# Optimization experiments

Measured on AMD Instinct MI355X. Metric: run time of the kernel, lower is better.

Reference implementation:

```python
import jax, jax.numpy as jnp
import numpy as np

N, C, L = 1024, 3, 6000
CONV_CH = [20, 32, 64, 20]
K = 3            # conv kernel size, padding (K-1)//2 = 1 -> SAME
POOL = 2
HID = 100
FLAT_DIM = (L // POOL**4 + 2 * C + 1) * CONV_CH[-1]  # (375 + 7) * 20 = 7640


def setup_inputs() -> dict:
    key = jax.random.key(0)
    ks = jax.random.split(key, 10)
    d = {"x": jax.random.normal(ks[0], (N, C, L), jnp.float32)}
    ins = [C] + CONV_CH[:-1]
    for i, (ic, oc) in enumerate(zip(ins, CONV_CH)):
        d[f"w{i}"] = jax.random.normal(ks[1 + i], (oc, ic, K), jnp.float32) * (1.0 / np.sqrt(ic * K))
        d[f"b{i}"] = jnp.zeros((oc,), jnp.float32)
    d["wc"] = jax.random.normal(ks[6], (CONV_CH[-1], C, 1), jnp.float32) * (1.0 / np.sqrt(C))
    d["bc"] = jnp.zeros((CONV_CH[-1],), jnp.float32)
    d["wl0"] = jax.random.normal(ks[7], (HID, FLAT_DIM), jnp.float32) * (1.0 / np.sqrt(FLAT_DIM))
    d["bl0"] = jnp.zeros((HID,), jnp.float32)
    d["wl1"] = jax.random.normal(ks[8], (2, HID), jnp.float32) * (1.0 / np.sqrt(HID))
    d["bl1"] = jnp.zeros((2,), jnp.float32)
    return d


def conv1d(x, w, b, pad):
    # x: (N, C_in, L), w: (C_out, C_in, K)
    out = jax.lax.conv_general_dilated(x, w, (1,), [(pad, pad)],
                                       dimension_numbers=('NCH', 'OIH', 'NCH'))
    return out + b[None, :, None]


def maxpool2(x):
    n, c, l = x.shape  # l always even here (6000 / 2^k)
    return x.reshape(n, c, l // 2, 2).max(-1)


def cov_eig_feats(x):
    # batched covariance as a single contraction (avoids the O(N*L*C*C) bmm intermediate)
    n, c, l = x.shape
    diff = x - x.mean(-1, keepdims=True)
    cov = jnp.einsum('ncl,ndl->ncd', diff, diff) / (l - 1)  # (N, C, C)
    # cov is symmetric PSD -> eigh (real); torch uses generic eig and keeps real parts
    vals, vecs = jnp.linalg.eigh(cov)
    vals = vals[..., None] / vals.max()          # global max over batch, like torch
    cov = cov / jnp.abs(cov).max()
    return jnp.concatenate([cov, vals, vecs], axis=-1)  # (N, C, 2C+1)


def reference(x, w0, b0, w1, b1, w2, b2, w3, b3, wc, bc, wl0, bl0, wl1, bl1):
    feats = jax.lax.stop_gradient(cov_eig_feats(x))  # torch branch is @no_grad
    h = x
    for w, b in ((w0, b0), (w1, b1), (w2, b2), (w3, b3)):
        h = maxpool2(jax.nn.relu(conv1d(h, w, b, (K - 1) // 2)))
    h = h.reshape(h.shape[0], -1)                    # (N, 20*375)
    h1 = jax.nn.relu(conv1d(feats, wc, bc, 0))       # (N, 20, 7)
    h1 = h1.reshape(h1.shape[0], -1)
    h = jnp.concatenate([h, h1], axis=1)             # (N, 7640)
    h = jax.nn.relu(h @ wl0.T + bl0)
    out = h @ wl1.T + bl1                            # (N, 2)
    return (out[:, :1], out[:, 1:])
```

## Files before the change

### kernel.cpp

```cpp
#include <hip/hip_runtime.h>
#include <hip/hip_bf16.h>
#include <hip/hip_fp16.h>
#include <math.h>

#define NBATCH 1024
#define LIN    6000
#define HCATW  7640
#define HID    100

#define TCH   54
#define NCHK  7

#define ASZ 3552
#define BSZ 7040

#define W0OFF 0
#define W1OFF 192
#define W2OFF 1472
#define W3OFF 5568
#define B0OFF 9664
#define B1OFF 9684
#define B2OFF 9716
#define B3OFF 9780
#define WREPSZ 9800

#define FCNS 4

typedef _Float16 v2h __attribute__((ext_vector_type(2)));

__device__ __forceinline__ float fdot2_f16(unsigned int a, unsigned int b, float c) {
#if __has_builtin(__builtin_amdgcn_fdot2)
    v2h ah, bh;
    __builtin_memcpy(&ah, &a, 4);
    __builtin_memcpy(&bh, &b, 4);
    return __builtin_amdgcn_fdot2(ah, bh, c, false);
#else
    float d;
    asm("v_dot2_f32_f16 %0, %1, %2, %3" : "=v"(d) : "v"(a), "v"(b), "v"(c));
    return d;
#endif
}

__device__ __forceinline__ void pack_one(int idx, int OC, int IC, int OCG,
                                         int OPG, int WSTR,
                                         const float* __restrict__ w,
                                         float* __restrict__ dst)
{
    if (idx >= OCG * IC * WSTR) return;
    int ocg = idx / (IC * WSTR);
    int r   = idx - ocg * (IC * WSTR);
    int ic  = r / WSTR;
    int q   = r - ic * WSTR;
    int o   = q / 3, k = q - o * 3;
    int oc  = ocg * OPG + o;
    dst[idx] = (o < OPG && oc < OC) ? w[(oc * IC + ic) * 3 + k] : 0.f;
}

__device__ __forceinline__ void pack_pk(int idx, int OC, int IC,
                                        const float* __restrict__ w,
                                        unsigned int* __restrict__ dst)
{
    const int OCG = OC >> 3;
    if (idx >= OCG * IC * 16) return;
    int ocg = idx / (IC * 16);
    int r   = idx - ocg * (IC * 16);
    int ic  = r >> 4, q = r & 15;
    int o   = q & 7;
    int oc  = ocg * 8 + o;
    const float* ws = w + (oc * IC + ic) * 3;
    if (q < 8) {
        unsigned int lo = __half_as_ushort(__float2half(ws[0]));
        unsigned int hi = __half_as_ushort(__float2half(ws[1]));
        dst[idx] = lo | (hi << 16);
    } else {
        dst[idx] = __float_as_uint(ws[2]);
    }
}

__global__ __launch_bounds__(256) void repack_kernel(
    const float* __restrict__ w0, const float* __restrict__ b0,
    const float* __restrict__ w1, const float* __restrict__ b1,
    const float* __restrict__ w2, const float* __restrict__ b2,
    const float* __restrict__ w3, const float* __restrict__ b3,
    float* __restrict__ wrep)
{
    int idx = blockIdx.x * 256 + threadIdx.x;
    unsigned int* wu = (unsigned int*)wrep;
    pack_one(idx, 20,  3, 4, 5, 16, w0, wrep + W0OFF);
    pack_pk (idx, 32, 20, w1, wu + W1OFF);
    pack_pk (idx, 64, 32, w2, wu + W2OFF);
    pack_one(idx, 20, 64, 4, 5, 16, w3, wrep + W3OFF);
    if (idx < 20)            wrep[B0OFF + idx] = b0[idx];
    else if (idx < 52)  { int i = idx - 20;  wrep[B1OFF + i] = b1[i]; }
    else if (idx < 116) { int i = idx - 52;  wrep[B2OFF + i] = b2[i]; }
    else if (idx < 136) { int i = idx - 116; wrep[B3OFF + i] = b3[i]; }
}

template<int IC, int OC, int OCG, int OPG, int WSTR, int JOUT, int LG, int JBLK,
         bool IN16, bool OUT16, bool PKW, bool FINAL>
__device__ __forceinline__ void stage_eo(const float* __restrict__ in,
                                         float* __restrict__ out,
                                         float* __restrict__ outg,
                                         const float* __restrict__ wrep,
                                         const float* __restrict__ brep,
                                         int pbase, int o3, int wv, int lane,
                                         int zero)
{
    constexpr int PIN  = JOUT + 1;
    constexpr int POUT = JOUT / 2;
    constexpr int NJT  = (JOUT + 64 * JBLK - 1) / (64 * JBLK);
    for (int task = wv; task < OCG * NJT; task += 8) {
        const int ocg = task / NJT;
        const int jt  = task - ocg * NJT;
        const int j0  = jt * (64 * JBLK) + lane;
        const float* bp = brep + ocg * OPG;
        float ae[JBLK][OPG], ao[JBLK][OPG];
#pragma unroll
        for (int t = 0; t < JBLK; ++t)
#pragma unroll
            for (int o = 0; o < OPG; ++o) { ae[t][o] = bp[o]; ao[t][o] = ae[t][o]; }
        const float* wbase = wrep + ocg * (IC * WSTR) + zero;
#pragma unroll 2
        for (int ic = 0; ic < IC; ++ic) {
            const float* wp = wbase + ic * WSTR;
            float wr[WSTR];
#pragma unroll
            for (int q = 0; q < WSTR / 4; ++q)
                *(float4*)&wr[q * 4] = *(const float4*)(wp + q * 4);
#pragma unroll
            for (int t = 0; t < JBLK; ++t) {
                const int jj = j0 + t * 64;
                const int jc = (jj < JOUT) ? jj : (JOUT - 1);
                if constexpr (PKW) {
                    const float* ipw = in + ic * PIN;
                    uint2 pw;
                    __builtin_memcpy(&pw, ipw + jc, 8);
                    const unsigned int crossu = (pw.x >> 16) | (pw.y << 16);
                    v2h h1; __builtin_memcpy(&h1, &pw.y, 4);
                    const float e1 = (float)h1.x, o1 = (float)h1.y;
#pragma unroll
                    for (int o = 0; o < OPG; ++o) {
                        const unsigned int wpk = __float_as_uint(wr[o]);
                        const float w2 = wr[8 + o];
                        ae[t][o] = fdot2_f16(pw.x,  wpk, ae[t][o]);
                        ao[t][o] = fdot2_f16(crossu, wpk, ao[t][o]);
                        ae[t][o] = fmaf(e1, w2, ae[t][o]);
                        ao[t][o] = fmaf(o1, w2, ao[t][o]);
                    }
                } else {
                    float e0, e1, o0, o1;
                    if constexpr (IN16) {
                        const float* ipw = in + ic * PIN;
                        uint2 pw;
                        __builtin_memcpy(&pw, ipw + jc, 8);
                        __half2 h0 = *reinterpret_cast<const __half2*>(&pw.x);
                        __half2 h1 = *reinterpret_cast<const __half2*>(&pw.y);
                        e0 = __low2float(h0); o0 = __high2float(h0);
                        e1 = __low2float(h1); o1 = __high2float(h1);
                    } else {
                        const float* ip = in + ic * (2 * PIN);
                        float2 ev, ov;
                        __builtin_memcpy(&ev, ip + jc, 8);
                        __builtin_memcpy(&ov, ip + PIN + jc, 8);
                        e0 = ev.x; e1 = ev.y;
                        o0 = ov.x; o1 = ov.y;
                    }
#pragma unroll
                    for (int o = 0; o < OPG; ++o) {
                        const float w0 = wr[o*3+0], w1 = wr[o*3+1], w2 = wr[o*3+2];
                        ae[t][o] = fmaf(e0, w0, fmaf(o0, w1, fmaf(e1, w2, ae[t][o])));
                        ao[t][o] = fmaf(o0, w0, fmaf(e1, w1, fmaf(o1, w2, ao[t][o])));
                    }
                }
            }
        }
#pragma unroll
        for (int t = 0; t < JBLK; ++t) {
            const int jj = j0 + t * 64;
            if constexpr (FINAL) {
                const int gj = o3 + jj;
                if (gj < 375 && jj < JOUT) {
#pragma unroll
                    for (int o = 0; o < OPG; ++o)
                        outg[(ocg*OPG+o) * 375 + gj] =
                            fmaxf(fmaxf(ae[t][o], ao[t][o]), 0.f);
                }
            } else {
                const int g = pbase + jj;
                const bool val = (jj < JOUT) && (g >= 0) && (g < LG);
                if (jj < JOUT) {
                    if constexpr (OUT16) {
                        __half* dh = (__half*)out;
#pragma unroll
                        for (int o = 0; o < OPG; ++o) {
                            float v = val ? fmaxf(fmaxf(ae[t][o], ao[t][o]), 0.f)
                                          : 0.f;
                            dh[(ocg*OPG+o) * JOUT + jj] = __float2half(v);
                        }
                    } else {
                        float* dst = out + ((jj & 1) ? POUT : 0) + (jj >> 1);
#pragma unroll
                        for (int o = 0; o < OPG; ++o)
                            dst[(ocg*OPG+o) * JOUT] =
                                val ? fmaxf(fmaxf(ae[t][o], ao[t][o]), 0.f) : 0.f;
                    }
                }
            }
        }
    }
}

__device__ __forceinline__ void stage3_split(const float* __restrict__ in,
                                             float* __restrict__ part,
                                             float* __restrict__ outg,
                                             const float* __restrict__ wrep,
                                             const float* __restrict__ brep,
                                             int o3, int wv, int lane, int zero)
{
    constexpr int JOUT = 54, PIN = 55, OPG = 5, WSTR = 16;
    const int ocg = wv & 3, ih = wv >> 2;
    const int j  = lane;
    const int jc = (j < JOUT) ? j : (JOUT - 1);
    const float* bp = brep + ocg * OPG;
    float ae[OPG], ao[OPG];
#pragma unroll
    for (int o = 0; o < OPG; ++o) {
        float b = ih ? 0.f : bp[o];
        ae[o] = b; ao[o] = b;
    }
    const float* wbase = wrep + (ocg * 64 + ih * 32) * WSTR + zero;
#pragma unroll 2
    for (int ic = 0; ic < 32; ++ic) {
        const float* ip = in + (ih * 32 + ic) * (2 * PIN);
        float2 ev, ov;
        __builtin_memcpy(&ev, ip + jc, 8);
        __builtin_memcpy(&ov, ip + PIN + jc, 8);
        const float* wp = wbase + ic * WSTR;
        float wr[WSTR];
#pragma unroll
        for (int q = 0; q < WSTR / 4; ++q)
            *(float4*)&wr[q * 4] = *(const float4*)(wp + q * 4);
#pragma unroll
        for (int o = 0; o < OPG; ++o) {
            const float w0 = wr[o*3+0], w1 = wr[o*3+1], w2 = wr[o*3+2];
            ae[o] = fmaf(ev.x, w0, fmaf(ov.x, w1, fmaf(ev.y, w2, ae[o])));
            ao[o] = fmaf(ov.x, w0, fmaf(ev.y, w1, fmaf(ov.y, w2, ao[o])));
        }
    }
    if (ih == 1) {
#pragma unroll
        for (int o = 0; o < OPG; ++o) {
            float2 p = make_float2(ae[o], ao[o]);
            __builtin_memcpy(part + (ocg * OPG + o) * 128 + lane * 2, &p, 8);
        }
    }
    __syncthreads();
    if (ih == 0) {
#pragma unroll
        for (int o = 0; o < OPG; ++o) {
            float2 p;
            __builtin_memcpy(&p, part + (ocg * OPG + o) * 128 + lane * 2, 8);
            ae[o] += p.x; ao[o] += p.y;
        }
        const int gj = o3 + j;
        if (gj < 375 && j < JOUT) {
#pragma unroll
            for (int o = 0; o < OPG; ++o)
                outg[(ocg * OPG + o) * 375 + gj] =
                    fmaxf(fmaxf(ae[o], ao[o]), 0.f);
        }
    }
}

__global__ __launch_bounds__(512, 6) void conv_chain_eo(
    const float* __restrict__ x,
    const float* __restrict__ wrep,
    float* __restrict__ hcat)
{
    __shared__ float A[ASZ];
    __shared__ float B[BSZ];

    const int tid  = threadIdx.x;
    const int wv   = __builtin_amdgcn_readfirstlane(tid >> 6);
    const int lane = tid & 63;
    const int zero = __builtin_amdgcn_ds_bpermute(0, 0);
    const int n     = blockIdx.x / NCHK;
    const int chunk = blockIdx.x % NCHK;
    const int o3 = chunk * TCH;
    const int p2 = 2*o3 - 1, p1 = 4*o3 - 3, p0 = 8*o3 - 7, xs = 16*o3 - 15;

    const float* xn = x + (size_t)n * 3 * LIN;
    for (int idx = tid; idx < 3 * 894; idx += 512) {
        int c = idx / 894, i = idx - c * 894;
        int g = xs + i;
        float v = (g >= 0 && g < LIN) ? xn[c * LIN + g] : 0.f;
        A[c * 894 + ((i & 1) ? 447 : 0) + (i >> 1)] = v;
    }
    __syncthreads();
    stage_eo< 3, 20, 4, 5, 16, 446, 3000, 2, false, true,  false, false>(
        A, B, nullptr, wrep + W0OFF, wrep + B0OFF, p0, o3, wv, lane, zero);
    __syncthreads();
    stage_eo<20, 32, 4, 8, 16, 222, 1500, 2, true,  true,  true,  false>(
        B, A, nullptr, wrep + W1OFF, wrep + B1OFF, p1, o3, wv, lane, zero);
    __syncthreads();
    stage_eo<32, 64, 8, 8, 16, 110,  750, 2, true,  false, true,  false>(
        A, B, nullptr, wrep + W2OFF, wrep + B2OFF, p2, o3, wv, lane, zero);
    __syncthreads();
    stage3_split(B, A, hcat + (size_t)n * HCATW,
                 wrep + W3OFF, wrep + B3OFF, o3, wv, lane, zero);
}

__device__ __forceinline__ float fsign(float a, float b) {
    return (b >= 0.0f) ? fabsf(a) : -fabsf(a);
}
__device__ __forceinline__ float slapy2(float xx, float yy) {
    float xa = fabsf(xx), ya = fabsf(yy);
    float w = fmaxf(xa, ya), z = fminf(xa, ya);
    if (z == 0.f) return w;
    float t = z / w;
    return w * sqrtf(1.f + t*t);
}
__device__ __forceinline__ void slartg(float f, float g, float& c, float& s, float& r) {
    if (g == 0.f)      { c = 1.f; s = 0.f; r = f; }
    else if (f == 0.f) { c = 0.f; s = (g >= 0.f ? 1.f : -1.f); r = fabsf(g); }
    else {
        float d = sqrtf(f*f + g*g);
        c = fabsf(f) / d;
        r = fsign(d, f);
        s = g / r;
    }
}
__device__ void slaev2(float a, float b, float cc,
                       float& rt1, float& rt2, float& cs1, float& sn1) {
    float sm = a + cc, df = a - cc;
    float adf = fabsf(df);
    float tb = b + b, ab = fabsf(tb);
    float acmx, acmn;
    if (fabsf(a) > fabsf(cc)) { acmx = a; acmn = cc; } else { acmx = cc; acmn = a; }
    float rt;
    if (adf > ab)      { float t = ab/adf; rt = adf*sqrtf(1.f + t*t); }
    else if (adf < ab) { float t = adf/ab; rt = ab*sqrtf(1.f + t*t); }
    else rt = ab * sqrtf(2.f);
    int sgn1;
    if (sm < 0.f)      { rt1 = 0.5f*(sm - rt); sgn1 = -1; rt2 = (acmx/rt1)*acmn - (b/rt1)*b; }
    else if (sm > 0.f) { rt1 = 0.5f*(sm + rt); sgn1 =  1; rt2 = (acmx/rt1)*acmn - (b/rt1)*b; }
    else               { rt1 = 0.5f*rt; rt2 = -0.5f*rt; sgn1 = 1; }
    float cs; int sgn2;
    if (df >= 0.f) { cs = df + rt; sgn2 = 1; } else { cs = df - rt; sgn2 = -1; }
    float acs = fabsf(cs);
    if (acs > ab) {
        float ct = -tb / cs;
        sn1 = 1.f / sqrtf(1.f + ct*ct);
        cs1 = ct * sn1;
    } else {
        if (ab == 0.f) { cs1 = 1.f; sn1 = 0.f; }
        else {
            float tn = -cs / tb;
            cs1 = 1.f / sqrtf(1.f + tn*tn);
            sn1 = tn * cs1;
        }
    }
    if (sgn1 == sgn2) { float tn = cs1; cs1 = -sn1; sn1 = tn; }
}
__device__ __forceinline__ void rot_cols(float z[3][3], int jc, float c, float s) {
    for (int i = 0; i < 3; ++i) {
        float t = z[i][jc+1];
        z[i][jc+1] = c*t - s*z[i][jc];
        z[i][jc]   = s*t + c*z[i][jc];
    }
}

__device__ void ssteqr3(float d[3], float e[2], float z[3][3]) {
    const float eps    = 5.9604645e-8f;
    const float eps2   = eps * eps;
    const float safmin = 1.17549435e-38f;
    const int n = 3;
    for (int i = 0; i < 3; ++i)
        for (int j = 0; j < 3; ++j) z[i][j] = (i == j) ? 1.f : 0.f;
    const int nmaxit = n * 30;
    int jtot = 0;
    float cw[2], sw[2];
    int l1 = 1, l, m, lend, lsv, lendsv;

L10:
    if (l1 > n) goto L160;
    if (l1 > 1) e[l1-2] = 0.f;
    if (l1 <= n-1) {
        for (m = l1; m <= n-1; ++m) {
            float tst = fabsf(e[m-1]);
            if (tst == 0.f) goto L30;
            if (tst <= (sqrtf(fabsf(d[m-1])) * sqrtf(fabsf(d[m]))) * eps) {
                e[m-1] = 0.f;
                goto L30;
            }
        }
    }
    m = n;
L30:
    l = l1; lsv = l; lend = m; lendsv = lend; l1 = m + 1;
    if (lend == l) goto L10;
    if (fabsf(d[lend-1]) < fabsf(d[l-1])) { lend = lsv; l = lendsv; }
    if (lend > l) {
L40:
        if (l != lend) {
            bool found = false;
            for (m = l; m <= lend-1; ++m) {
                float tst = e[m-1]*e[m-1];
                if (tst <= (eps2*fabsf(d[m-1]))*fabsf(d[m]) + safmin) { found = true; break; }
            }
            if (!found) m = lend;
        } else m = lend;
        if (m < lend) e[m-1] = 0.f;
        {
            float p = d[l-1];
            if (m == l) {
                d[l-1] = p;
                l = l + 1;
                if (l <= lend) goto L40;
                goto L140;
            }
            if (m == l+1) {
                float rt1, rt2, c2, s2;
                slaev2(d[l-1], e[l-1], d[l], rt1, rt2, c2, s2);
                rot_cols(z, l-1, c2, s2);
                d[l-1] = rt1; d[l] = rt2; e[l-1] = 0.f;
                l += 2;
                if (l <= lend) goto L40;
                goto L140;
            }
            if (jtot == nmaxit) goto L140;
            jtot++;
            float g = (d[l] - p) / (2.f * e[l-1]);
            float r = slapy2(g, 1.f);
            g = d[m-1] - p + e[l-1] / (g + fsign(r, g));
            float s = 1.f, c = 1.f;
            p = 0.f;
            for (int i = m-1; i >= l; --i) {
                float f = s * e[i-1];
                float b = c * e[i-1];
                slartg(g, f, c, s, r);
                if (i != m-1) e[i] = r;
                g = d[i] - p;
                r = (d[i-1] - g)*s + 2.f*c*b;
                p = s * r;
                d[i] = g + p;
                g = c*r - b;
                cw[i-l] = c; sw[i-l] = -s;
            }
            for (int jj = m-l; jj >= 1; --jj)
                rot_cols(z, l + jj - 2, cw[jj-1], sw[jj-1]);
            d[l-1] = d[l-1] - p;
            e[l-1] = g;
            goto L40;
        }
    } else {
L90:
        if (l != lend) {
            bool found = false;
            for (m = l; m >= lend+1; --m) {
                float tst = e[m-2]*e[m-2];
                if (tst <= (eps2*fabsf(d[m-1]))*fabsf(d[m-2]) + safmin) { found = true; break; }
            }
            if (!found) m = lend;
        } else m = lend;
        if (m > lend) e[m-2] = 0.f;
        {
            float p = d[l-1];
            if (m == l) {
                d[l-1] = p;
                l = l - 1;
                if (l >= lend) goto L90;
                goto L140;
            }
            if (m == l-1) {
                float rt1, rt2, c2, s2;
                slaev2(d[l-2], e[l-2], d[l-1], rt1, rt2, c2, s2);
                rot_cols(z, l-2, c2, s2);
                d[l-2] = rt1; d[l-1] = rt2; e[l-2] = 0.f;
                l -= 2;
                if (l >= lend) goto L90;
                goto L140;
            }
            if (jtot == nmaxit) goto L140;
            jtot++;
            float g = (d[l-2] - p) / (2.f * e[l-2]);
            float r = slapy2(g, 1.f);
            g = d[m-1] - p + e[l-2] / (g + fsign(r, g));
            float s = 1.f, c = 1.f;
            p = 0.f;
            for (int i = m; i <= l-1; ++i) {
                float f = s * e[i-1];
                float b = c * e[i-1];
                slartg(g, f, c, s, r);
                if (i != m) e[i-2] = r;
                g = d[i-1] - p;
                r = (d[i] - g)*s + 2.f*c*b;
                p = s * r;
                d[i-1] = g + p;
                g = c*r - b;
                cw[i-m] = c; sw[i-m] = s;
            }
            for (int jj = 1; jj <= l-m; ++jj)
                rot_cols(z, m + jj - 2, cw[jj-1], sw[jj-1]);
            d[l-1] = d[l-1] - p;
            e[l-2] = g;
            goto L90;
        }
    }
L140:
    if (jtot < nmaxit) goto L10;
L160:
    for (int ii = 2; ii <= n; ++ii) {
        int i = ii - 1, k = i;
        float p = d[i-1];
        for (int j = ii; j <= n; ++j)
            if (d[j-1] < p) { k = j; p = d[j-1]; }
        if (k != i) {
            d[k-1] = d[i-1]; d[i-1] = p;
            for (int r0 = 0; r0 < 3; ++r0) {
                float t = z[r0][i-1]; z[r0][i-1] = z[r0][k-1]; z[r0][k-1] = t;
            }
        }
    }
}

__global__ __launch_bounds__(256) void cov_eig_kernel(const float* __restrict__ x,
                                                      float* __restrict__ eigbuf,
                                                      unsigned int* __restrict__ gmax)
{
    __shared__ float part[4][9];
    const int n = blockIdx.x;
    const float* xn = x + (size_t)n * 3 * LIN;
    float v[9] = {0,0,0,0,0,0,0,0,0};
    for (int l = threadIdx.x; l < LIN; l += 256) {
        float a = xn[l], b = xn[LIN + l], c = xn[2*LIN + l];
        v[0] += a; v[1] += b; v[2] += c;
        v[3] = fmaf(a,a,v[3]); v[4] = fmaf(a,b,v[4]); v[5] = fmaf(a,c,v[5]);
        v[6] = fmaf(b,b,v[6]); v[7] = fmaf(b,c,v[7]); v[8] = fmaf(c,c,v[8]);
    }
#pragma unroll
    for (int off = 32; off > 0; off >>= 1)
#pragma unroll
        for (int i = 0; i < 9; ++i) v[i] += __shfl_down(v[i], off, 64);
    const int wv = threadIdx.x >> 6, lane = threadIdx.x & 63;
    if (lane == 0)
        for (int i = 0; i < 9; ++i) part[wv][i] = v[i];
    __syncthreads();
    if (threadIdx.x == 0) {
        float t[9];
        for (int i = 0; i < 9; ++i)
            t[i] = part[0][i] + part[1][i] + part[2][i] + part[3][i];
        const float Lf = (float)LIN;
        float m0 = t[0]/Lf, m1 = t[1]/Lf, m2 = t[2]/Lf;
        float c00 = (t[3] - Lf*m0*m0) / (Lf - 1.f);
        float c01 = (t[4] - Lf*m0*m1) / (Lf - 1.f);
        float c02 = (t[5] - Lf*m0*m2) / (Lf - 1.f);
        float c11 = (t[6] - Lf*m1*m1) / (Lf - 1.f);
        float c12 = (t[7] - Lf*m1*m2) / (Lf - 1.f);
        float c22 = (t[8] - Lf*m2*m2) / (Lf - 1.f);

        float dd[3], ee[2], tau, v2;
        {
            float a21 = c01, a31 = c02, a22 = c11, a32 = c12, a33 = c22;
            float xnorm = fabsf(a31);
            if (xnorm == 0.f) {
                tau = 0.f; v2 = 0.f;
                dd[0] = c00; dd[1] = a22; dd[2] = a33;
                ee[0] = a21; ee[1] = a32;
            } else {
                float beta = -fsign(slapy2(a21, xnorm), a21);
                tau = (beta - a21) / beta;
                v2  = a31 / (a21 - beta);
                ee[0] = beta;
                float x1 = tau*(a22 + a32*v2);
                float x2 = tau*(a32 + a33*v2);
                float al = -0.5f*tau*(x1 + x2*v2);
                float w1 = x1 + al;
                float w2 = x2 + al*v2;
                a22 -= 2.f*w1;
                a32 -= (v2*w1 + w2);
                a33 -= 2.f*v2*w2;
                dd[0] = c00; dd[1] = a22; dd[2] = a33;
                ee[1] = a32;
            }
        }
        float zz[3][3];
        ssteqr3(dd, ee, zz);
        if (tau != 0.f) {
            for (int j = 0; j < 3; ++j) {
                float sum = zz[1][j] + v2*zz[2][j];
                zz[1][j] -= tau * sum;
                zz[2][j] -= tau * v2 * sum;
            }
        }

        float* eb = eigbuf + n * 21;
        eb[0] = c00; eb[1] = c01; eb[2] = c02;
        eb[3] = c01; eb[4] = c11; eb[5] = c12;
        eb[6] = c02; eb[7] = c12; eb[8] = c22;
        eb[9] = dd[0]; eb[10] = dd[1]; eb[11] = dd[2];
        for (int c = 0; c < 3; ++c)
            for (int k = 0; k < 3; ++k) eb[12 + c*3 + k] = zz[c][k];

        float vmax = fmaxf(dd[0], fmaxf(dd[1], dd[2]));
        float cmax = 0.f;
        for (int i = 0; i < 9; ++i) cmax = fmaxf(cmax, fabsf(eb[i]));
        atomicMax(&gmax[0], __float_as_uint(vmax));
        atomicMax(&gmax[1], __float_as_uint(cmax));
    }
}

__global__ __launch_bounds__(256) void feats_kernel(const float* __restrict__ eigbuf,
                                                    const unsigned int* __restrict__ gmax,
                                                    const float* __restrict__ wc,
                                                    const float* __restrict__ bc,
                                                    float* __restrict__ hcat)
{
    const int n = blockIdx.x;
    const int t = threadIdx.x;
    if (t >= 140) return;
    const int o = t / 7, j = t % 7;
    const float* eb = eigbuf + n * 21;
    const float vmax = __uint_as_float(gmax[0]);
    const float cmax = __uint_as_float(gmax[1]);
    float f0, f1, f2;
    if (j < 3)       { f0 = eb[0*3+j]/cmax; f1 = eb[1*3+j]/cmax; f2 = eb[2*3+j]/cmax; }
    else if (j == 3) { f0 = eb[9]/vmax;     f1 = eb[10]/vmax;    f2 = eb[11]/vmax; }
    else             { int k = j-4; f0 = eb[12+0*3+k]; f1 = eb[12+1*3+k]; f2 = eb[12+2*3+k]; }
    float r = bc[o] + wc[o*3+0]*f0 + wc[o*3+1]*f1 + wc[o*3+2]*f2;
    hcat[(size_t)n*HCATW + 7500 + o*7 + j] = fmaxf(r, 0.f);
}

__global__ __launch_bounds__(512) void fc01_kernel(const float* __restrict__ hcat,
                                                   const float* __restrict__ wl0,
                                                   const float* __restrict__ bl0,
                                                   const float* __restrict__ wl1,
                                                   const float* __restrict__ bl1,
                                                   float* __restrict__ out)
{
    __shared__ float hl[FCNS * HCATW];
    __shared__ float hbuf[FCNS * HID];
    const int tid = threadIdx.x;
    const int n0 = blockIdx.x * FCNS;
    for (int i = tid; i < FCNS * (HCATW/4); i += 512) {
        int s  = i / (HCATW/4);
        int k4 = i - s * (HCATW/4);
        ((float4*)hl)[s * (HCATW/4) + k4] =
            *(const float4*)(hcat + (size_t)(n0 + s) * HCATW + k4 * 4);
    }
    __syncthreads();
    const int wv = tid >> 6;
    const int lane = tid & 63;
    for (int ot = wv; ot < HID / 4; ot += 8) {
        float acc[4][FCNS];
#pragma unroll
        for (int oo = 0; oo < 4; ++oo)
#pragma unroll
            for (int s = 0; s < FCNS; ++s) acc[oo][s] = 0.f;
        for (int k = lane * 4; k < HCATW; k += 256) {
            float4 hv[FCNS];
#pragma unroll
            for (int s = 0; s < FCNS; ++s)
                hv[s] = *(const float4*)(hl + s * HCATW + k);
#pragma unroll
            for (int oo = 0; oo < 4; ++oo) {
                const float4 w4 = *(const float4*)(wl0 + (size_t)(ot*4+oo) * HCATW + k);
#pragma unroll
                for (int s = 0; s < FCNS; ++s) {
                    acc[oo][s] = fmaf(hv[s].x, w4.x, acc[oo][s]);
                    acc[oo][s] = fmaf(hv[s].y, w4.y, acc[oo][s]);
                    acc[oo][s] = fmaf(hv[s].z, w4.z, acc[oo][s]);
                    acc[oo][s] = fmaf(hv[s].w, w4.w, acc[oo][s]);
                }
            }
        }
#pragma unroll
        for (int off = 32; off > 0; off >>= 1)
#pragma unroll
            for (int oo = 0; oo < 4; ++oo)
#pragma unroll
                for (int s = 0; s < FCNS; ++s)
                    acc[oo][s] += __shfl_down(acc[oo][s], off, 64);
        if (lane == 0) {
#pragma unroll
            for (int oo = 0; oo < 4; ++oo) {
                const float b = bl0[ot*4+oo];
#pragma unroll
                for (int s = 0; s < FCNS; ++s)
                    hbuf[s * HID + ot*4+oo] = fmaxf(acc[oo][s] + b, 0.f);
            }
        }
    }
    __syncthreads();
    if (tid < 2 * FCNS) {
        const int s = tid >> 1, r = tid & 1;
        const float* w = wl1 + r * HID;
        float acc = bl1[r];
        for (int k = 0; k < HID; ++k) acc = fmaf(hbuf[s * HID + k], w[k], acc);
        out[r * NBATCH + n0 + s] = acc;
    }
}

extern "C" void kernel_launch(void* const* d_in, const int* in_sizes, int n_in,
                              void* d_out, int out_size, void* d_ws, size_t ws_size,
                              hipStream_t stream)
{
    const float* x   = (const float*)d_in[0];
    const float* w0  = (const float*)d_in[1];
    const float* b0  = (const float*)d_in[2];
    const float* w1  = (const float*)d_in[3];
    const float* b1  = (const float*)d_in[4];
    const float* w2  = (const float*)d_in[5];
    const float* b2  = (const float*)d_in[6];
    const float* w3  = (const float*)d_in[7];
    const float* b3  = (const float*)d_in[8];
    const float* wc  = (const float*)d_in[9];
    const float* bc  = (const float*)d_in[10];
    const float* wl0 = (const float*)d_in[11];
    const float* bl0 = (const float*)d_in[12];
    const float* wl1 = (const float*)d_in[13];
    const float* bl1 = (const float*)d_in[14];
    float* out = (float*)d_out;

    const size_t HCAT_N = (size_t)NBATCH * HCATW;
    const size_t EIG_N  = (size_t)NBATCH * 21;
    const size_t need_bytes = (HCAT_N + EIG_N + 4 + WREPSZ) * 4 + 16;
    if (ws_size < need_bytes) return;

    float* ws     = (float*)d_ws;
    float* hcat   = ws;
    float* eigbuf = hcat + HCAT_N;
    unsigned int* gmax = (unsigned int*)(eigbuf + EIG_N);
    float* wrep   = (float*)(gmax + 4);

    hipMemsetAsync(gmax, 0, 2 * sizeof(unsigned int), stream);

    repack_kernel<<<16, 256, 0, stream>>>(w0, b0, w1, b1, w2, b2, w3, b3, wrep);
    conv_chain_eo<<<NBATCH * NCHK, 512, 0, stream>>>(x, wrep, hcat);
    cov_eig_kernel<<<NBATCH, 256, 0, stream>>>(x, eigbuf, gmax);
    feats_kernel<<<NBATCH, 256, 0, stream>>>(eigbuf, gmax, wc, bc, hcat);
    fc01_kernel<<<NBATCH / FCNS, 512, 0, stream>>>(hcat, wl0, bl0, wl1, bl1, out);
}
```

Before: 652.0 us.

## Use fp16 packed dot products for conv stage 3 and FC layer

Stage 2 now writes its output as packed fp16 into a smaller shared buffer, and stage 3 reads packed halves and uses v_dot2 with fp16-packed weights. The FC1 weights are converted to fp16 by a new per-call kernel, and the hidden activations are staged in shared memory as fp16. Batch rows per FC block double, so each weight load is reused across more samples. The smaller shared footprint lets the occupancy hint rise to 8 blocks per CU, at the cost of reduced precision in these layers.

Result: faster. 615.4 us (-5.6%).

```diff
diff --git a/kernel.cpp b/kernel.cpp
--- a/kernel.cpp
+++ b/kernel.cpp
@@ -12,7 +12,7 @@
 #define NCHK  7
 
 #define ASZ 3552
-#define BSZ 7040
+#define BSZ 4460
 
 #define W0OFF 0
 #define W1OFF 192
@@ -24,7 +24,9 @@
 #define B3OFF 9780
 #define WREPSZ 9800
 
-#define FCNS 4
+#define WL0HSZ (HID * (HCATW/2))
+
+#define FCNS 8
 
 typedef _Float16 v2h __attribute__((ext_vector_type(2)));
 
@@ -56,25 +58,29 @@
     dst[idx] = (o < OPG && oc < OC) ? w[(oc * IC + ic) * 3 + k] : 0.f;
 }
 
-__device__ __forceinline__ void pack_pk(int idx, int OC, int IC,
+__device__ __forceinline__ void pack_pk(int idx, int OC, int IC, int OCG, int OPG,
                                         const float* __restrict__ w,
                                         unsigned int* __restrict__ dst)
 {
-    const int OCG = OC >> 3;
     if (idx >= OCG * IC * 16) return;
     int ocg = idx / (IC * 16);
     int r   = idx - ocg * (IC * 16);
     int ic  = r >> 4, q = r & 15;
     int o   = q & 7;
-    int oc  = ocg * 8 + o;
-    const float* ws = w + (oc * IC + ic) * 3;
-    if (q < 8) {
-        unsigned int lo = __half_as_ushort(__float2half(ws[0]));
-        unsigned int hi = __half_as_ushort(__float2half(ws[1]));
-        dst[idx] = lo | (hi << 16);
-    } else {
-        dst[idx] = __float_as_uint(ws[2]);
-    }
+    int oc  = ocg * OPG + o;
+    bool valid = (o < OPG) && (oc < OC);
+    unsigned int v = 0;
+    if (valid) {
+        const float* ws = w + (oc * IC + ic) * 3;
+        if (q < 8) {
+            unsigned int lo = __half_as_ushort(__float2half(ws[0]));
+            unsigned int hi = __half_as_ushort(__float2half(ws[1]));
+            v = lo | (hi << 16);
+        } else {
+            v = __float_as_uint(ws[2]);
+        }
+    }
+    dst[idx] = v;
 }
 
 __global__ __launch_bounds__(256) void repack_kernel(
@@ -87,13 +93,24 @@
     int idx = blockIdx.x * 256 + threadIdx.x;
     unsigned int* wu = (unsigned int*)wrep;
     pack_one(idx, 20,  3, 4, 5, 16, w0, wrep + W0OFF);
-    pack_pk (idx, 32, 20, w1, wu + W1OFF);
-    pack_pk (idx, 64, 32, w2, wu + W2OFF);
-    pack_one(idx, 20, 64, 4, 5, 16, w3, wrep + W3OFF);
+    pack_pk (idx, 32, 20, 4, 8, w1, wu + W1OFF);
+    pack_pk (idx, 64, 32, 8, 8, w2, wu + W2OFF);
+    pack_pk (idx, 20, 64, 4, 5, w3, wu + W3OFF);
     if (idx < 20)            wrep[B0OFF + idx] = b0[idx];
     else if (idx < 52)  { int i = idx - 20;  wrep[B1OFF + i] = b1[i]; }
     else if (idx < 116) { int i = idx - 52;  wrep[B2OFF + i] = b2[i]; }
     else if (idx < 136) { int i = idx - 116; wrep[B3OFF + i] = b3[i]; }
+}
+
+__global__ __launch_bounds__(256) void wl0h_kernel(const float* __restrict__ wl0,
+                                                   unsigned int* __restrict__ wl0h)
+{
+    int idx = blockIdx.x * 256 + threadIdx.x;
+    if (idx >= WL0HSZ) return;
+    float a = wl0[idx * 2], b = wl0[idx * 2 + 1];
+    unsigned int lo = __half_as_ushort(__float2half(a));
+    unsigned int hi = __half_as_ushort(__float2half(b));
+    wl0h[idx] = lo | (hi << 16);
 }
 
 template<int IC, int OC, int OCG, int OPG, int WSTR, int JOUT, int LG, int JBLK,
@@ -217,7 +234,7 @@
                                              const float* __restrict__ brep,
                                              int o3, int wv, int lane, int zero)
 {
-    constexpr int JOUT = 54, PIN = 55, OPG = 5, WSTR = 16;
+    constexpr int JOUT = 54, PIND = 55, OPG = 5, WSTR = 16;
     const int ocg = wv & 3, ih = wv >> 2;
     const int j  = lane;
     const int jc = (j < JOUT) ? j : (JOUT - 1);
@@ -231,10 +248,12 @@
     const float* wbase = wrep + (ocg * 64 + ih * 32) * WSTR + zero;
 #pragma unroll 2
     for (int ic = 0; ic < 32; ++ic) {
-        const float* ip = in + (ih * 32 + ic) * (2 * PIN);
-        float2 ev, ov;
-        __builtin_memcpy(&ev, ip + jc, 8);
-        __builtin_memcpy(&ov, ip + PIN + jc, 8);
+        const float* ipw = in + (ih * 32 + ic) * PIND;
+        uint2 pw;
+        __builtin_memcpy(&pw, ipw + jc, 8);
+        const unsigned int crossu = (pw.x >> 16) | (pw.y << 16);
+        v2h h1; __builtin_memcpy(&h1, &pw.y, 4);
+        const float e1 = (float)h1.x, o1 = (float)h1.y;
         const float* wp = wbase + ic * WSTR;
         float wr[WSTR];
 #pragma unroll
@@ -242,9 +261,12 @@
             *(float4*)&wr[q * 4] = *(const float4*)(wp + q * 4);
 #pragma unroll
         for (int o = 0; o < OPG; ++o) {
-            const float w0 = wr[o*3+0], w1 = wr[o*3+1], w2 = wr[o*3+2];
-            ae[o] = fmaf(ev.x, w0, fmaf(ov.x, w1, fmaf(ev.y, w2, ae[o])));
-            ao[o] = fmaf(ov.x, w0, fmaf(ev.y, w1, fmaf(ov.y, w2, ao[o])));
+            const unsigned int wpk = __float_as_uint(wr[o]);
+            const float w2 = wr[8 + o];
+            ae[o] = fdot2_f16(pw.x,   wpk, ae[o]);
+            ao[o] = fdot2_f16(crossu, wpk, ao[o]);
+            ae[o] = fmaf(e1, w2, ae[o]);
+            ao[o] = fmaf(o1, w2, ao[o]);
         }
     }
     if (ih == 1) {
@@ -272,7 +294,7 @@
     }
 }
 
-__global__ __launch_bounds__(512, 6) void conv_chain_eo(
+__global__ __launch_bounds__(512, 8) void conv_chain_eo(
     const float* __restrict__ x,
     const float* __restrict__ wrep,
     float* __restrict__ hcat)
@@ -303,7 +325,7 @@
     stage_eo<20, 32, 4, 8, 16, 222, 1500, 2, true,  true,  true,  false>(
         B, A, nullptr, wrep + W1OFF, wrep + B1OFF, p1, o3, wv, lane, zero);
     __syncthreads();
-    stage_eo<32, 64, 8, 8, 16, 110,  750, 2, true,  false, true,  false>(
+    stage_eo<32, 64, 8, 8, 16, 110,  750, 2, true,  true,  true,  false>(
         A, B, nullptr, wrep + W2OFF, wrep + B2OFF, p2, o3, wv, lane, zero);
     __syncthreads();
     stage3_split(B, A, hcat + (size_t)n * HCATW,
@@ -632,21 +654,24 @@
 }
 
 __global__ __launch_bounds__(512) void fc01_kernel(const float* __restrict__ hcat,
-                                                   const float* __restrict__ wl0,
+                                                   const unsigned int* __restrict__ wl0h,
                                                    const float* __restrict__ bl0,
                                                    const float* __restrict__ wl1,
                                                    const float* __restrict__ bl1,
                                                    float* __restrict__ out)
 {
-    __shared__ float hl[FCNS * HCATW];
+    __shared__ __half hl[FCNS * HCATW];
     __shared__ float hbuf[FCNS * HID];
     const int tid = threadIdx.x;
     const int n0 = blockIdx.x * FCNS;
     for (int i = tid; i < FCNS * (HCATW/4); i += 512) {
         int s  = i / (HCATW/4);
         int k4 = i - s * (HCATW/4);
-        ((float4*)hl)[s * (HCATW/4) + k4] =
-            *(const float4*)(hcat + (size_t)(n0 + s) * HCATW + k4 * 4);
+        float4 v = *(const float4*)(hcat + (size_t)(n0 + s) * HCATW + k4 * 4);
+        __half2 h01 = __floats2half2_rn(v.x, v.y);
+        __half2 h23 = __floats2half2_rn(v.z, v.w);
+        *(__half2*)(hl + s * HCATW + k4 * 4)     = h01;
+        *(__half2*)(hl + s * HCATW + k4 * 4 + 2) = h23;
     }
     __syncthreads();
     const int wv = tid >> 6;
@@ -657,20 +682,22 @@
         for (int oo = 0; oo < 4; ++oo)
 #pragma unroll
             for (int s = 0; s < FCNS; ++s) acc[oo][s] = 0.f;
-        for (int k = lane * 4; k < HCATW; k += 256) {
-            float4 hv[FCNS];
+        for (int k = lane * 8; k < HCATW; k += 512) {
+            uint4 hv[FCNS];
 #pragma unroll
             for (int s = 0; s < FCNS; ++s)
-                hv[s] = *(const float4*)(hl + s * HCATW + k);
+                hv[s] = *(const uint4*)(hl + s * HCATW + k);
 #pragma unroll
             for (int oo = 0; oo < 4; ++oo) {
-                const float4 w4 = *(const float4*)(wl0 + (size_t)(ot*4+oo) * HCATW + k);
+                const uint4 wp = *(const uint4*)(wl0h + (ot*4+oo) * (HCATW/2) + (k >> 1));
 #pragma unroll
                 for (int s = 0; s < FCNS; ++s) {
-                    acc[oo][s] = fmaf(hv[s].x, w4.x, acc[oo][s]);
-                    acc[oo][s] = fmaf(hv[s].y, w4.y, acc[oo][s]);
-                    acc[oo][s] = fmaf(hv[s].z, w4.z, acc[oo][s]);
-                    acc[oo][s] = fmaf(hv[s].w, w4.w, acc[oo][s]);
+                    float a = acc[oo][s];
+                    a = fdot2_f16(hv[s].x, wp.x, a);
+                    a = fdot2_f16(hv[s].y, wp.y, a);
+                    a = fdot2_f16(hv[s].z, wp.z, a);
+                    a = fdot2_f16(hv[s].w, wp.w, a);
+                    acc[oo][s] = a;
                 }
             }
         }
@@ -724,7 +751,7 @@
 
     const size_t HCAT_N = (size_t)NBATCH * HCATW;
     const size_t EIG_N  = (size_t)NBATCH * 21;
-    const size_t need_bytes = (HCAT_N + EIG_N + 4 + WREPSZ) * 4 + 16;
+    const size_t need_bytes = (HCAT_N + EIG_N + 4 + WREPSZ + WL0HSZ) * 4 + 16;
     if (ws_size < need_bytes) return;
 
     float* ws     = (float*)d_ws;
@@ -732,12 +759,14 @@
     float* eigbuf = hcat + HCAT_N;
     unsigned int* gmax = (unsigned int*)(eigbuf + EIG_N);
     float* wrep   = (float*)(gmax + 4);
+    unsigned int* wl0h = (unsigned int*)(wrep + WREPSZ);
 
     hipMemsetAsync(gmax, 0, 2 * sizeof(unsigned int), stream);
 
     repack_kernel<<<16, 256, 0, stream>>>(w0, b0, w1, b1, w2, b2, w3, b3, wrep);
+    wl0h_kernel<<<(WL0HSZ + 255) / 256, 256, 0, stream>>>(wl0, wl0h);
     conv_chain_eo<<<NBATCH * NCHK, 512, 0, stream>>>(x, wrep, hcat);
     cov_eig_kernel<<<NBATCH, 256, 0, stream>>>(x, eigbuf, gmax);
     feats_kernel<<<NBATCH, 256, 0, stream>>>(eigbuf, gmax, wc, bc, hcat);
-    fc01_kernel<<<NBATCH / FCNS, 512, 0, stream>>>(hcat, wl0, bl0, wl1, bl1, out);
-}
+    fc01_kernel<<<NBATCH / FCNS, 512, 0, stream>>>(hcat, wl0h, bl0, wl1, bl1, out);
+}
```
